# Kernel optimization log

Hardware: AMD Instinct MI355X
Metric: run time of the kernel (lower is better)

The kernel has to match this reference:

```python
import jax, jax.numpy as jnp
import numpy as np

NQ = 16  # nqubits
BATCH = 256

def _ry(t):
    # t: (...,) real angles -> (..., 2, 2) complex64 Ry(t)
    c = jnp.cos(t / 2).astype(jnp.complex64)
    s = jnp.sin(t / 2).astype(jnp.complex64)
    return jnp.stack([jnp.stack([c, -s], -1), jnp.stack([s, c], -1)], -2)

def _rz(t):
    # diag(e^{-i t/2}, e^{i t/2})
    e0 = jnp.exp(-0.5j * t.astype(jnp.complex64))
    e1 = jnp.exp(0.5j * t.astype(jnp.complex64))
    z = jnp.zeros_like(e0)
    return jnp.stack([jnp.stack([e0, z], -1), jnp.stack([z, e1], -1)], -2)

def _apply_1q(st, g, w):
    # st: (B, 2^n) complex, g: (2,2) or (B,2,2); wire w (0 = most significant, matching kron order)
    B = st.shape[0]
    x = st.reshape(B, 2 ** w, 2, -1)
    if g.ndim == 3:
        x = jnp.einsum('iab,ilbr->ilar', g, x)
    else:
        x = jnp.einsum('ab,ilbr->ilar', g, x)
    return x.reshape(B, -1)

def _apply_cnot(st, c, t, n):
    # CNOT(control=c, target=t): flip target bit where control bit == 1
    B = st.shape[0]
    x = st.reshape((B,) + (2,) * n)
    c_ax = c + 1
    ctrl0 = jnp.take(x, 0, axis=c_ax)
    ctrl1 = jnp.take(x, 1, axis=c_ax)
    t_ax = t + 1 if t < c else t  # target axis index after removing control axis
    ctrl1 = jnp.flip(ctrl1, axis=t_ax)  # flip along size-2 axis == Pauli-X
    x = jnp.stack([ctrl0, ctrl1], axis=c_ax)
    return x.reshape(B, -1)

def _yzy(st, w3, n):
    # per-qubit Ry(a) Rz(b) Ry(c); params laid out (n, 3) applied in order a, b, c
    p = w3.reshape(n, 3)
    g = jnp.einsum('nab,nbc,ncd->nad', _ry(p[:, 2]), _rz(p[:, 1]), _ry(p[:, 0]))
    for i in range(n):
        st = _apply_1q(st, g[i], i)
    return st

def _ring(st, step, n):
    # ring_of_cnot (step=1) / ring_of_cnot2 (step=2)
    for i in range(n):
        st = _apply_cnot(st, i, (i + step) % n, n)
    return st

def _forward(inputs, weight):
    B, n = inputs.shape
    # |0...0> initial state, batched
    st = jnp.zeros((B, 2 ** n), jnp.complex64).at[:, 0].set(1.0)
    # PauliEncoding with pauli='Y': Ry(inputs[:, i]) on wire i (batched gate)
    enc = _ry(inputs)  # (B, n, 2, 2)
    for i in range(n):
        st = _apply_1q(st, enc[:, i], i)
    # BasicEntangleLayer x2 = YZY + ring_of_cnot
    st = _yzy(st, weight[0 * n:3 * n], n); st = _ring(st, 1, n)
    st = _yzy(st, weight[3 * n:6 * n], n); st = _ring(st, 1, n)
    # YZY, ring_of_cnot2, YZY, ring_of_cnot2, YZY
    st = _yzy(st, weight[6 * n:9 * n], n); st = _ring(st, 2, n)
    st = _yzy(st, weight[9 * n:12 * n], n); st = _ring(st, 2, n)
    st = _yzy(st, weight[12 * n:15 * n], n)
    # <Z_i> = sum_probs(bit_i=0) - sum_probs(bit_i=1); output scaled by 4 as in original
    probs = st.real ** 2 + st.imag ** 2  # (B, 2^n) real
    z = []
    for i in range(n):
        p = probs.reshape(B, 2 ** i, 2, -1)
        z.append((p[:, :, 0, :] - p[:, :, 1, :]).sum(axis=(1, 2)))
    return jnp.stack(z, axis=1) * 4.0  # (B, n)

def setup_inputs() -> dict:
    key = jax.random.key(0)
    k1, k2 = jax.random.split(key)
    inputs = jax.random.uniform(k1, (BATCH, NQ), jnp.float32, 0.0, 2.0 * np.pi)
    weight = jax.random.uniform(k2, (15 * NQ,), jnp.float32, 0.0, 2.0 * np.pi)
    return {"inputs": inputs, "weight": weight}

def reference(inputs, weight):
    return _forward(inputs, weight)
```

## Files before the change

### kernel.cpp

```cpp
#include <hip/hip_runtime.h>
#include <hip/hip_fp16.h>
#include <utility>
#include <type_traits>


struct M16 { unsigned r[16]; };

constexpr M16 ident() { M16 m{}; for (int i = 0; i < 16; ++i) m.r[i] = 1u << i; return m; }

constexpr M16 ringm(int s) {
  M16 m = ident();
  for (int i = 15; i >= 0; --i) {
    int pc = 15 - i;
    int pt = 15 - ((i + s) & 15);
    m.r[pt] ^= m.r[pc];
  }
  return m;
}

constexpr M16 mmul(M16 A, M16 B) {
  M16 C{};
  for (int p = 0; p < 16; ++p) {
    unsigned v = 0;
    for (int q = 0; q < 16; ++q) if ((A.r[p] >> q) & 1u) v ^= B.r[q];
    C.r[p] = v;
  }
  return C;
}

constexpr M16 minv(M16 A) {
  M16 I = ident();
  for (int col = 0; col < 16; ++col) {
    int piv = -1;
    for (int row = col; row < 16; ++row) if ((A.r[row] >> col) & 1u) { piv = row; break; }
    unsigned t = A.r[piv]; A.r[piv] = A.r[col]; A.r[col] = t;
    t = I.r[piv]; I.r[piv] = I.r[col]; I.r[col] = t;
    for (int row = 0; row < 16; ++row)
      if (row != col && ((A.r[row] >> col) & 1u)) { A.r[row] ^= A.r[col]; I.r[row] ^= I.r[col]; }
  }
  return I;
}

constexpr bool meq(M16 a, M16 b) { for (int i = 0; i < 16; ++i) if (a.r[i] != b.r[i]) return false; return true; }
constexpr unsigned colmask(M16 P, int b) { unsigned m = 0; for (int p = 0; p < 16; ++p) m |= ((P.r[p] >> b) & 1u) << p; return m; }
constexpr int popc16(unsigned x) { int c = 0; for (int i = 0; i < 16; ++i) c += (x >> i) & 1; return c; }
constexpr int topbit_pow(unsigned x) { int b = 0; for (int i = 0; i < 16; ++i) if ((x >> i) & 1) b = i; return 1 << b; }

struct Tables { unsigned gm[64]; unsigned gc[64]; unsigned meas[16]; };

constexpr Tables make_tables() {
  Tables T{};
  M16 R1 = ringm(1), R2 = ringm(2);
  M16 P0 = R1;
  M16 P1 = mmul(R1, R1);
  M16 P2 = mmul(P1, R2);
  M16 P3 = mmul(P2, R2);
  M16 P[4] = { P0, P1, P2, P3 };
  for (int k = 0; k < 4; ++k) {
    M16 A = minv(P[k]);
    for (int b = 0; b < 16; ++b) {
      T.gm[k * 16 + b] = colmask(P[k], b);
      T.gc[k * 16 + b] = A.r[b];
    }
  }
  M16 A5 = minv(P[3]);
  for (int w = 0; w < 16; ++w) T.meas[w] = A5.r[15 - w];
  return T;
}

constexpr Tables TB = make_tables();

constexpr bool check_tables() {
  for (int g = 0; g < 64; ++g) if ((popc16(TB.gm[g] & TB.gc[g]) & 1) != 1) return false;
  if (!meq(mmul(ringm(1), minv(ringm(1))), ident())) return false;
  if (!meq(mmul(ringm(2), minv(ringm(2))), ident())) return false;
  return true;
}
static_assert(check_tables(), "GF(2) table inconsistency");
static_assert(sizeof(__half2) == 4, "half2 size");

template<int N, int I = 0, typename F>
__device__ __forceinline__ void sfor(F&& f) {
  if constexpr (I < N) {
    f(std::integral_constant<int, I>{});
    sfor<N, I + 1>(static_cast<F&&>(f));
  }
}

__device__ __forceinline__ int h2i(__half2 v) { return __builtin_bit_cast(int, v); }
__device__ __forceinline__ __half2 i2h(int v) { return __builtin_bit_cast(__half2, v); }
__device__ __forceinline__ unsigned h2u(__half2 v) { return __builtin_bit_cast(unsigned, v); }
__device__ __forceinline__ __half2 u2h(unsigned v) { return __builtin_bit_cast(__half2, v); }

__device__ __forceinline__ __half2 hswap(__half2 v) { __half2 r; r.x = v.y; r.y = v.x; return r; }

__device__ __forceinline__ __half2 updc(__half2 xs, __half2 xp, const __half2 (&s)[4]) {
  __half2 y = __hmul2(s[0], xs);
  y = __hfma2(s[1], hswap(xs), y);
  y = __hfma2(s[2], xp, y);
  y = __hfma2(s[3], hswap(xp), y);
  return y;
}
template<int T>
__device__ __forceinline__ __half2 upd(__half2 xs, __half2 xp,
                                       const __half2 (&s0)[4], const __half2 (&s1)[4]) {
  if constexpr (T) return updc(xs, xp, s1); else return updc(xs, xp, s0);
}

__device__ __forceinline__ void su2_coeffs(float a, float b, float c,
                                           float& are, float& aim, float& bre, float& bim) {
  float sapc, capc, samc, camc, sb, cb;
  __sincosf((a + c) * 0.5f, &sapc, &capc);
  __sincosf((a - c) * 0.5f, &samc, &camc);
  __sincosf(b * 0.5f, &sb, &cb);
  are = cb * capc;
  aim = -sb * camc;
  bre = cb * sapc;
  bim = sb * samc;
}

__device__ __forceinline__ unsigned pkh2(float lo, float hi) {
  return h2u(__floats2half2_rn(lo, hi));
}

__device__ __forceinline__ float2 cmulf(float2 a, float vr, float vi) {
  return make_float2(a.x * vr - a.y * vi, a.x * vi + a.y * vr);
}

template<int G>
__device__ __forceinline__ void apply_gate(__half2 (&S)[64], unsigned tid,
                                           const unsigned* ctab, unsigned* xbuf) {
  constexpr unsigned m  = TB.gm[G];
  constexpr unsigned c  = TB.gc[G];
  constexpr unsigned mL = m & 63u;
  constexpr unsigned mT = m >> 6;
  constexpr unsigned mW = m >> 12;
  constexpr int      dt = popc16(c & mL) & 1;

  __half2 s0[4], s1[4];
  {
    const unsigned f = __popc((c >> 6) & tid) & 1u;
#pragma unroll
    for (int q = 0; q < 4; ++q) {
      const unsigned lo = ctab[G * 8 + q];
      const unsigned hi = ctab[G * 8 + 4 + q];
      s0[q] = u2h(f ? hi : lo);
      s1[q] = u2h(f ? lo : hi);
    }
  }

  if constexpr (mT == 0u) {
    static_assert(mT != 0u || dt == 1, "register-pair gate must flip role locally");
    constexpr int hb = topbit_pow(mL);
    sfor<32>([&](auto ii) {
      constexpr int i  = decltype(ii)::value;
      constexpr int L0 = ((i & ~(hb - 1)) << 1) | (i & (hb - 1));
      constexpr int L1 = L0 ^ (int)mL;
      constexpr int t  = popc16(c & (unsigned)L0) & 1;
      const __half2 x0 = S[L0], x1 = S[L1];
      S[L0] = upd<t>(x0, x1, s0, s1);
      S[L1] = upd<t ^ dt>(x1, x0, s0, s1);
    });
  } else if constexpr (mW == 0u) {
    if constexpr (mL == 0u) {
      sfor<64>([&](auto ll) {
        constexpr int L = decltype(ll)::value;
        constexpr int t = popc16(c & (unsigned)L) & 1;
        const __half2 xp = i2h(__shfl_xor(h2i(S[L]), (int)mT, 64));
        S[L] = upd<t>(S[L], xp, s0, s1);
      });
    } else {
      constexpr int hb = topbit_pow(mL);
      sfor<32>([&](auto ii) {
        constexpr int i  = decltype(ii)::value;
        constexpr int L0 = ((i & ~(hb - 1)) << 1) | (i & (hb - 1));
        constexpr int L1 = L0 ^ (int)mL;
        constexpr int t  = popc16(c & (unsigned)L0) & 1;
        const __half2 x0 = S[L0], x1 = S[L1];
        const __half2 xp0 = i2h(__shfl_xor(h2i(x1), (int)mT, 64));
        const __half2 xp1 = i2h(__shfl_xor(h2i(x0), (int)mT, 64));
        S[L0] = upd<t>(x0, xp0, s0, s1);
        S[L1] = upd<t ^ dt>(x1, xp1, s0, s1);
      });
    }
  } else {
    constexpr unsigned hc = mL >> 3;
    const unsigned ptid = tid ^ mT;
    if constexpr (hc == 0u) {
      sfor<4>([&](auto gg_) {
        constexpr int g = decltype(gg_)::value;
        sfor<16>([&](auto ss) {
          constexpr int s = decltype(ss)::value;
          xbuf[s * 1024 + tid] = h2u(S[g * 16 + s]);
        });
        __syncthreads();
        sfor<16>([&](auto ss) {
          constexpr int s    = decltype(ss)::value;
          constexpr int L    = g * 16 + s;
          constexpr int slot = (L ^ (int)mL) & 15;
          constexpr int t    = popc16(c & (unsigned)L) & 1;
          const __half2 xp = u2h(xbuf[slot * 1024 + ptid]);
          S[L] = upd<t>(S[L], xp, s0, s1);
        });
        __syncthreads();
      });
    } else {
      constexpr int tb = topbit_pow(hc);
      sfor<8>([&](auto cc) {
        constexpr int cA = decltype(cc)::value;
        if constexpr ((cA & tb) == 0) {
          constexpr int cB = cA ^ (int)hc;
          sfor<8>([&](auto ss) {
            constexpr int s = decltype(ss)::value;
            xbuf[s * 1024 + tid]       = h2u(S[cA * 8 + s]);
            xbuf[(8 + s) * 1024 + tid] = h2u(S[cB * 8 + s]);
          });
          __syncthreads();
          sfor<8>([&](auto ss) {
            constexpr int s = decltype(ss)::value;
            {
              constexpr int L    = cA * 8 + s;
              constexpr int slot = 8 + ((L ^ (int)mL) & 7);
              constexpr int t    = popc16(c & (unsigned)L) & 1;
              const __half2 xp = u2h(xbuf[slot * 1024 + ptid]);
              S[L] = upd<t>(S[L], xp, s0, s1);
            }
            {
              constexpr int L    = cB * 8 + s;
              constexpr int slot = (L ^ (int)mL) & 7;
              constexpr int t    = popc16(c & (unsigned)L) & 1;
              const __half2 xp = u2h(xbuf[slot * 1024 + ptid]);
              S[L] = upd<t>(S[L], xp, s0, s1);
            }
          });
          __syncthreads();
        }
      });
    }
  }
}

__global__ __attribute__((amdgpu_flat_work_group_size(1024, 1024),
                          amdgpu_waves_per_eu(4, 4)))
void qcir_kernel(const float* __restrict__ inputs, const float* __restrict__ weight,
                 float* __restrict__ out) {
  __shared__ unsigned xbuf[24 * 1024];
  __shared__ unsigned ctab[64 * 8];
  __shared__ float4   itab[16];
  __shared__ float    red[16 * 16];

  const unsigned tid = threadIdx.x;
  const unsigned b   = blockIdx.x;

  if (tid < 64) {
    const int g = (int)tid;
    const int k = g >> 4;
    const int bb = g & 15;
    const int w = 15 - bb;
    const int base = 48 * (k + 1) + 3 * w;
    float are, aim, bre, bim;
    su2_coeffs(weight[base], weight[base + 1], weight[base + 2], are, aim, bre, bim);
    ctab[g * 8 + 0] = pkh2(are, are);
    ctab[g * 8 + 1] = pkh2(-aim, aim);
    ctab[g * 8 + 2] = pkh2(-bre, -bre);
    ctab[g * 8 + 3] = pkh2(-bim, bim);
    ctab[g * 8 + 4] = pkh2(are, are);
    ctab[g * 8 + 5] = pkh2(aim, -aim);
    ctab[g * 8 + 6] = pkh2(bre, bre);
    ctab[g * 8 + 7] = pkh2(-bim, bim);
  } else if (tid < 80) {
    const int w = (int)tid - 64;
    const float a = weight[3 * w] + inputs[b * 16 + w];
    float are, aim, bre, bim;
    su2_coeffs(a, weight[3 * w + 1], weight[3 * w + 2], are, aim, bre, bim);
    itab[w] = make_float4(are, aim, bre, bim);
  }
  __syncthreads();

  __half2 S[64];
  float2 P = make_float2(1.f, 0.f);
#pragma unroll
  for (int p = 6; p <= 15; ++p) {
    const int bit = (int)(tid >> (p - 6)) & 1;
    const float4 t = itab[15 - p];
    P = cmulf(P, bit ? t.z : t.x, bit ? t.w : t.y);
  }
  sfor<8>([&](auto hh) {
    constexpr int h = decltype(hh)::value;
    float2 ph = P;
    sfor<3>([&](auto qq) {
      constexpr int q   = decltype(qq)::value;
      constexpr int bit = (h >> q) & 1;
      const float4 t = itab[15 - (3 + q)];
      if constexpr (bit) ph = cmulf(ph, t.z, t.w); else ph = cmulf(ph, t.x, t.y);
    });
    sfor<8>([&](auto ll) {
      constexpr int l = decltype(ll)::value;
      float2 pl = ph;
      sfor<3>([&](auto qq) {
        constexpr int q   = decltype(qq)::value;
        constexpr int bit = (l >> q) & 1;
        const float4 t = itab[15 - q];
        if constexpr (bit) pl = cmulf(pl, t.z, t.w); else pl = cmulf(pl, t.x, t.y);
      });
      S[h * 8 + l] = __floats2half2_rn(pl.x, pl.y);
    });
  });

  sfor<64>([&](auto gg) { apply_gate<decltype(gg)::value>(S, tid, ctab, xbuf); });

  float acc[16];
  sfor<16>([&](auto ww) { acc[decltype(ww)::value] = 0.f; });
  sfor<64>([&](auto ll) {
    constexpr int L = decltype(ll)::value;
    const float re = __low2float(S[L]);
    const float im = __high2float(S[L]);
    const float p = re * re + im * im;
    sfor<16>([&](auto ww) {
      constexpr int w = decltype(ww)::value;
      constexpr int t = popc16(TB.meas[w] & 63u & (unsigned)L) & 1;
      if constexpr (t) acc[w] -= p; else acc[w] += p;
    });
  });
  sfor<16>([&](auto ww) {
    constexpr int w = decltype(ww)::value;
    const unsigned fw = __popc((TB.meas[w] >> 6) & tid) & 1u;
    float z = fw ? -acc[w] : acc[w];
#pragma unroll
    for (int d = 1; d < 64; d <<= 1) z += __shfl_xor(z, d, 64);
    if ((tid & 63u) == 0u) red[(tid >> 6) * 16 + w] = z;
  });
  __syncthreads();
  if (tid < 16) {
    float s = 0.f;
#pragma unroll
    for (int v = 0; v < 16; ++v) s += red[v * 16 + tid];
    out[b * 16 + tid] = 4.f * s;
  }
}

extern "C" void kernel_launch(void* const* d_in, const int* in_sizes, int n_in,
                              void* d_out, int out_size, void* d_ws, size_t ws_size,
                              hipStream_t stream) {
  const float* inputs = (const float*)d_in[0];
  const float* weight = (const float*)d_in[1];
  float* out = (float*)d_out;
  const int B = in_sizes[0] / 16;
  qcir_kernel<<<B, 1024, 0, stream>>>(inputs, weight, out);
}
```

Baseline: 338.8 us.

## Keep 48 amplitudes in registers and spill the last 16 to LDS

The per-thread state drops from 64 register half2 amplitudes to 48. The remaining 16 live in a per-thread LDS region accessed with 128-bit vector loads and stores, and every gate path is extended to handle the LDS-resident part. The gate coefficients shrink to one uint4 per gate, with a sign-flip mask applied by XOR instead of selecting between two coefficient sets. The aim is to cut register pressure and spilling at 1024 threads per block, paid for with extra LDS traffic on every gate.

New measurement: 356.0 us. 5.1% more time.

```diff
diff --git a/kernel.cpp b/kernel.cpp
--- a/kernel.cpp
+++ b/kernel.cpp
@@ -3,6 +3,8 @@
 #include <utility>
 #include <type_traits>
 
+
+constexpr int NREG = 48;
 
 struct M16 { unsigned r[16]; };
 
@@ -94,17 +96,16 @@
 
 __device__ __forceinline__ __half2 hswap(__half2 v) { __half2 r; r.x = v.y; r.y = v.x; return r; }
 
-__device__ __forceinline__ __half2 updc(__half2 xs, __half2 xp, const __half2 (&s)[4]) {
-  __half2 y = __hmul2(s[0], xs);
-  y = __hfma2(s[1], hswap(xs), y);
-  y = __hfma2(s[2], xp, y);
-  y = __hfma2(s[3], hswap(xp), y);
-  return y;
-}
 template<int T>
 __device__ __forceinline__ __half2 upd(__half2 xs, __half2 xp,
-                                       const __half2 (&s0)[4], const __half2 (&s1)[4]) {
-  if constexpr (T) return updc(xs, xp, s1); else return updc(xs, xp, s0);
+                                       __half2 c0, __half2 c1, __half2 c2, __half2 c3) {
+  __half2 c1t = c1, c2t = c2;
+  if constexpr (T) { c1t = __hneg2(c1); c2t = __hneg2(c2); }
+  __half2 y = __hmul2(c0, xs);
+  y = __hfma2(c1t, hswap(xs), y);
+  y = __hfma2(c2t, xp, y);
+  y = __hfma2(c3, hswap(xp), y);
+  return y;
 }
 
 __device__ __forceinline__ void su2_coeffs(float a, float b, float c,
@@ -127,9 +128,72 @@
   return make_float2(a.x * vr - a.y * vi, a.x * vi + a.y * vr);
 }
 
+template<int g4>
+__device__ __forceinline__ void ldg(const uint4* slds4, unsigned tid, __half2 (&a)[4]) {
+  const uint4 v = slds4[g4 * 1024 + tid];
+  a[0] = u2h(v.x); a[1] = u2h(v.y); a[2] = u2h(v.z); a[3] = u2h(v.w);
+}
+template<int g4>
+__device__ __forceinline__ void stg(uint4* slds4, unsigned tid, const __half2 (&a)[4]) {
+  slds4[g4 * 1024 + tid] = make_uint4(h2u(a[0]), h2u(a[1]), h2u(a[2]), h2u(a[3]));
+}
+
+template<int ch, int sb, int NR>
+__device__ __forceinline__ void stage_chunk(const __half2 (&S)[NR], unsigned tid,
+                                            const uint4* slds4, unsigned* xbuf) {
+  if constexpr (ch < 6) {
+    sfor<8>([&](auto kk) {
+      constexpr int k = decltype(kk)::value;
+      xbuf[(sb + k) * 1024 + tid] = h2u(S[ch * 8 + k]);
+    });
+  } else {
+    sfor<2>([&](auto uu) {
+      constexpr int u = decltype(uu)::value;
+      __half2 a[4];
+      ldg<(ch - 6) * 2 + u>(slds4, tid, a);
+      sfor<4>([&](auto ee) {
+        constexpr int e = decltype(ee)::value;
+        xbuf[(sb + u * 4 + e) * 1024 + tid] = h2u(a[e]);
+      });
+    });
+  }
+}
+
+template<int ch, int pb, unsigned mLt, unsigned ct, int NR>
+__device__ __forceinline__ void compute_chunk(__half2 (&S)[NR], unsigned tid, unsigned ptid,
+                                              uint4* slds4, const unsigned* xbuf,
+                                              __half2 c0, __half2 c1, __half2 c2, __half2 c3) {
+  if constexpr (ch < 6) {
+    sfor<8>([&](auto kk) {
+      constexpr int k = decltype(kk)::value;
+      constexpr int L = ch * 8 + k;
+      constexpr int slot = pb + ((L ^ (int)mLt) & 7);
+      constexpr int t = popc16(ct & (unsigned)L) & 1;
+      const __half2 xp = u2h(xbuf[slot * 1024 + ptid]);
+      S[L] = upd<t>(S[L], xp, c0, c1, c2, c3);
+    });
+  } else {
+    sfor<2>([&](auto uu) {
+      constexpr int u = decltype(uu)::value;
+      constexpr int g = (ch - 6) * 2 + u;
+      __half2 a[4];
+      ldg<g>(slds4, tid, a);
+      sfor<4>([&](auto ee) {
+        constexpr int e = decltype(ee)::value;
+        constexpr int L = ch * 8 + u * 4 + e;
+        constexpr int slot = pb + ((L ^ (int)mLt) & 7);
+        constexpr int t = popc16(ct & (unsigned)L) & 1;
+        const __half2 xp = u2h(xbuf[slot * 1024 + ptid]);
+        a[e] = upd<t>(a[e], xp, c0, c1, c2, c3);
+      });
+      stg<g>(slds4, tid, a);
+    });
+  }
+}
+
 template<int G>
-__device__ __forceinline__ void apply_gate(__half2 (&S)[64], unsigned tid,
-                                           const unsigned* ctab, unsigned* xbuf) {
+__device__ __forceinline__ void apply_gate(__half2 (&S)[NREG], unsigned tid,
+                                           const uint4* ctab4, uint4* slds4, unsigned* xbuf) {
   constexpr unsigned m  = TB.gm[G];
   constexpr unsigned c  = TB.gc[G];
   constexpr unsigned mL = m & 63u;
@@ -137,37 +201,106 @@
   constexpr unsigned mW = m >> 12;
   constexpr int      dt = popc16(c & mL) & 1;
 
-  __half2 s0[4], s1[4];
+  __half2 c0, c1, c2, c3;
   {
-    const unsigned f = __popc((c >> 6) & tid) & 1u;
-#pragma unroll
-    for (int q = 0; q < 4; ++q) {
-      const unsigned lo = ctab[G * 8 + q];
-      const unsigned hi = ctab[G * 8 + 4 + q];
-      s0[q] = u2h(f ? hi : lo);
-      s1[q] = u2h(f ? lo : hi);
-    }
-  }
+    const uint4 cc = ctab4[G];
+    const unsigned fm = (__popc((c >> 6) & tid) & 1u) ? 0x80008000u : 0u;
+    c0 = u2h(cc.x); c1 = u2h(cc.y ^ fm); c2 = u2h(cc.z ^ fm); c3 = u2h(cc.w);
+  }
+
+  constexpr unsigned dq = (mL >> 4) & 3u;
+  constexpr unsigned mn = mL & 15u;
 
   if constexpr (mT == 0u) {
-    static_assert(mT != 0u || dt == 1, "register-pair gate must flip role locally");
+    static_assert(dt == 1, "local pair gate must flip role");
     constexpr int hb = topbit_pow(mL);
     sfor<32>([&](auto ii) {
       constexpr int i  = decltype(ii)::value;
       constexpr int L0 = ((i & ~(hb - 1)) << 1) | (i & (hb - 1));
       constexpr int L1 = L0 ^ (int)mL;
-      constexpr int t  = popc16(c & (unsigned)L0) & 1;
-      const __half2 x0 = S[L0], x1 = S[L1];
-      S[L0] = upd<t>(x0, x1, s0, s1);
-      S[L1] = upd<t ^ dt>(x1, x0, s0, s1);
-    });
+      if constexpr (L0 < NREG && L1 < NREG) {
+        constexpr int t = popc16(c & (unsigned)L0) & 1;
+        const __half2 x0 = S[L0], x1 = S[L1];
+        S[L0] = upd<t>(x0, x1, c0, c1, c2, c3);
+        S[L1] = upd<t ^ dt>(x1, x0, c0, c1, c2, c3);
+      }
+    });
+    if constexpr (dq == 0u) {
+      constexpr unsigned hg = mn >> 2;
+      if constexpr (hg == 0u) {
+        constexpr int eb = topbit_pow(mn);
+        sfor<4>([&](auto gg4) {
+          constexpr int g = decltype(gg4)::value;
+          __half2 a[4]; ldg<g>(slds4, tid, a);
+          sfor<2>([&](auto jj) {
+            constexpr int j  = decltype(jj)::value;
+            constexpr int e0 = ((j & ~(eb - 1)) << 1) | (j & (eb - 1));
+            constexpr int e1 = e0 ^ (int)mn;
+            constexpr int L0 = 48 + g * 4 + e0;
+            constexpr int t  = popc16(c & (unsigned)L0) & 1;
+            const __half2 x0 = a[e0], x1 = a[e1];
+            a[e0] = upd<t>(x0, x1, c0, c1, c2, c3);
+            a[e1] = upd<t ^ dt>(x1, x0, c0, c1, c2, c3);
+          });
+          stg<g>(slds4, tid, a);
+        });
+      } else {
+        constexpr int gb = topbit_pow(hg);
+        sfor<2>([&](auto jj) {
+          constexpr int j  = decltype(jj)::value;
+          constexpr int gA = ((j & ~(gb - 1)) << 1) | (j & (gb - 1));
+          constexpr int gB = gA ^ (int)hg;
+          __half2 a[4], bb[4];
+          ldg<gA>(slds4, tid, a); ldg<gB>(slds4, tid, bb);
+          sfor<4>([&](auto ee) {
+            constexpr int e  = decltype(ee)::value;
+            constexpr int e2 = e ^ (int)(mn & 3u);
+            constexpr int L0 = 48 + gA * 4 + e;
+            constexpr int t  = popc16(c & (unsigned)L0) & 1;
+            const __half2 x0 = a[e], x1 = bb[e2];
+            a[e]   = upd<t>(x0, x1, c0, c1, c2, c3);
+            bb[e2] = upd<t ^ dt>(x1, x0, c0, c1, c2, c3);
+          });
+          stg<gA>(slds4, tid, a); stg<gB>(slds4, tid, bb);
+        });
+      }
+    } else {
+      constexpr int qr = 3 ^ (int)dq;
+      sfor<4>([&](auto gg4) {
+        constexpr int g = decltype(gg4)::value;
+        __half2 a[4]; ldg<g>(slds4, tid, a);
+        sfor<4>([&](auto ee) {
+          constexpr int e  = decltype(ee)::value;
+          constexpr int s  = g * 4 + e;
+          constexpr int Lr = (qr << 4) | (s ^ (int)mn);
+          static_assert(Lr < NREG, "reg partner must be register-resident");
+          constexpr int tr = popc16(c & (unsigned)Lr) & 1;
+          const __half2 xr = S[Lr], xl = a[e];
+          S[Lr] = upd<tr>(xr, xl, c0, c1, c2, c3);
+          a[e]  = upd<tr ^ dt>(xl, xr, c0, c1, c2, c3);
+        });
+        stg<g>(slds4, tid, a);
+      });
+    }
   } else if constexpr (mW == 0u) {
     if constexpr (mL == 0u) {
-      sfor<64>([&](auto ll) {
+      sfor<NREG>([&](auto ll) {
         constexpr int L = decltype(ll)::value;
         constexpr int t = popc16(c & (unsigned)L) & 1;
         const __half2 xp = i2h(__shfl_xor(h2i(S[L]), (int)mT, 64));
-        S[L] = upd<t>(S[L], xp, s0, s1);
+        S[L] = upd<t>(S[L], xp, c0, c1, c2, c3);
+      });
+      sfor<4>([&](auto gg4) {
+        constexpr int g = decltype(gg4)::value;
+        __half2 a[4]; ldg<g>(slds4, tid, a);
+        sfor<4>([&](auto ee) {
+          constexpr int e = decltype(ee)::value;
+          constexpr int L = 48 + g * 4 + e;
+          constexpr int t = popc16(c & (unsigned)L) & 1;
+          const __half2 xp = i2h(__shfl_xor(h2i(a[e]), (int)mT, 64));
+          a[e] = upd<t>(a[e], xp, c0, c1, c2, c3);
+        });
+        stg<g>(slds4, tid, a);
       });
     } else {
       constexpr int hb = topbit_pow(mL);
@@ -175,64 +308,138 @@
         constexpr int i  = decltype(ii)::value;
         constexpr int L0 = ((i & ~(hb - 1)) << 1) | (i & (hb - 1));
         constexpr int L1 = L0 ^ (int)mL;
-        constexpr int t  = popc16(c & (unsigned)L0) & 1;
-        const __half2 x0 = S[L0], x1 = S[L1];
-        const __half2 xp0 = i2h(__shfl_xor(h2i(x1), (int)mT, 64));
-        const __half2 xp1 = i2h(__shfl_xor(h2i(x0), (int)mT, 64));
-        S[L0] = upd<t>(x0, xp0, s0, s1);
-        S[L1] = upd<t ^ dt>(x1, xp1, s0, s1);
-      });
+        if constexpr (L0 < NREG && L1 < NREG) {
+          constexpr int t = popc16(c & (unsigned)L0) & 1;
+          const __half2 x0 = S[L0], x1 = S[L1];
+          const __half2 xp0 = i2h(__shfl_xor(h2i(x1), (int)mT, 64));
+          const __half2 xp1 = i2h(__shfl_xor(h2i(x0), (int)mT, 64));
+          S[L0] = upd<t>(x0, xp0, c0, c1, c2, c3);
+          S[L1] = upd<t ^ dt>(x1, xp1, c0, c1, c2, c3);
+        }
+      });
+      if constexpr (dq == 0u) {
+        constexpr unsigned hg = mn >> 2;
+        if constexpr (hg == 0u) {
+          constexpr int eb = topbit_pow(mn);
+          sfor<4>([&](auto gg4) {
+            constexpr int g = decltype(gg4)::value;
+            __half2 a[4]; ldg<g>(slds4, tid, a);
+            sfor<2>([&](auto jj) {
+              constexpr int j  = decltype(jj)::value;
+              constexpr int e0 = ((j & ~(eb - 1)) << 1) | (j & (eb - 1));
+              constexpr int e1 = e0 ^ (int)mn;
+              constexpr int L0 = 48 + g * 4 + e0;
+              constexpr int t  = popc16(c & (unsigned)L0) & 1;
+              const __half2 x0 = a[e0], x1 = a[e1];
+              const __half2 xp0 = i2h(__shfl_xor(h2i(x1), (int)mT, 64));
+              const __half2 xp1 = i2h(__shfl_xor(h2i(x0), (int)mT, 64));
+              a[e0] = upd<t>(x0, xp0, c0, c1, c2, c3);
+              a[e1] = upd<t ^ dt>(x1, xp1, c0, c1, c2, c3);
+            });
+            stg<g>(slds4, tid, a);
+          });
+        } else {
+          constexpr int gb = topbit_pow(hg);
+          sfor<2>([&](auto jj) {
+            constexpr int j  = decltype(jj)::value;
+            constexpr int gA = ((j & ~(gb - 1)) << 1) | (j & (gb - 1));
+            constexpr int gB = gA ^ (int)hg;
+            __half2 a[4], bb[4];
+            ldg<gA>(slds4, tid, a); ldg<gB>(slds4, tid, bb);
+            sfor<4>([&](auto ee) {
+              constexpr int e  = decltype(ee)::value;
+              constexpr int e2 = e ^ (int)(mn & 3u);
+              constexpr int L0 = 48 + gA * 4 + e;
+              constexpr int t  = popc16(c & (unsigned)L0) & 1;
+              const __half2 x0 = a[e], x1 = bb[e2];
+              const __half2 xp0 = i2h(__shfl_xor(h2i(x1), (int)mT, 64));
+              const __half2 xp1 = i2h(__shfl_xor(h2i(x0), (int)mT, 64));
+              a[e]   = upd<t>(x0, xp0, c0, c1, c2, c3);
+              bb[e2] = upd<t ^ dt>(x1, xp1, c0, c1, c2, c3);
+            });
+            stg<gA>(slds4, tid, a); stg<gB>(slds4, tid, bb);
+          });
+        }
+      } else {
+        constexpr int qr = 3 ^ (int)dq;
+        sfor<4>([&](auto gg4) {
+          constexpr int g = decltype(gg4)::value;
+          __half2 a[4]; ldg<g>(slds4, tid, a);
+          sfor<4>([&](auto ee) {
+            constexpr int e  = decltype(ee)::value;
+            constexpr int s  = g * 4 + e;
+            constexpr int Lr = (qr << 4) | (s ^ (int)mn);
+            static_assert(Lr < NREG, "reg partner must be register-resident");
+            constexpr int tr = popc16(c & (unsigned)Lr) & 1;
+            const __half2 xr = S[Lr], xl = a[e];
+            const __half2 xpr = i2h(__shfl_xor(h2i(xl), (int)mT, 64));
+            const __half2 xpl = i2h(__shfl_xor(h2i(xr), (int)mT, 64));
+            S[Lr] = upd<tr>(xr, xpr, c0, c1, c2, c3);
+            a[e]  = upd<tr ^ dt>(xl, xpl, c0, c1, c2, c3);
+          });
+          stg<g>(slds4, tid, a);
+        });
+      }
     }
   } else {
+    const unsigned ptid = tid ^ mT;
     constexpr unsigned hc = mL >> 3;
-    const unsigned ptid = tid ^ mT;
     if constexpr (hc == 0u) {
       sfor<4>([&](auto gg_) {
         constexpr int g = decltype(gg_)::value;
-        sfor<16>([&](auto ss) {
-          constexpr int s = decltype(ss)::value;
-          xbuf[s * 1024 + tid] = h2u(S[g * 16 + s]);
-        });
+        if constexpr (g < 3) {
+          sfor<16>([&](auto ss) {
+            constexpr int s = decltype(ss)::value;
+            xbuf[s * 1024 + tid] = h2u(S[g * 16 + s]);
+          });
+        } else {
+          sfor<4>([&](auto grr) {
+            constexpr int gr = decltype(grr)::value;
+            __half2 a[4]; ldg<gr>(slds4, tid, a);
+            sfor<4>([&](auto ee) {
+              constexpr int e = decltype(ee)::value;
+              xbuf[(gr * 4 + e) * 1024 + tid] = h2u(a[e]);
+            });
+          });
+        }
         __syncthreads();
-        sfor<16>([&](auto ss) {
-          constexpr int s    = decltype(ss)::value;
-          constexpr int L    = g * 16 + s;
-          constexpr int slot = (L ^ (int)mL) & 15;
-          constexpr int t    = popc16(c & (unsigned)L) & 1;
-          const __half2 xp = u2h(xbuf[slot * 1024 + ptid]);
-          S[L] = upd<t>(S[L], xp, s0, s1);
-        });
+        if constexpr (g < 3) {
+          sfor<16>([&](auto ss) {
+            constexpr int s    = decltype(ss)::value;
+            constexpr int L    = g * 16 + s;
+            constexpr int slot = (L ^ (int)mL) & 15;
+            constexpr int t    = popc16(c & (unsigned)L) & 1;
+            const __half2 xp = u2h(xbuf[slot * 1024 + ptid]);
+            S[L] = upd<t>(S[L], xp, c0, c1, c2, c3);
+          });
+        } else {
+          sfor<4>([&](auto grr) {
+            constexpr int gr = decltype(grr)::value;
+            __half2 a[4]; ldg<gr>(slds4, tid, a);
+            sfor<4>([&](auto ee) {
+              constexpr int e    = decltype(ee)::value;
+              constexpr int L    = 48 + gr * 4 + e;
+              constexpr int slot = (L ^ (int)mL) & 15;
+              constexpr int t    = popc16(c & (unsigned)L) & 1;
+              const __half2 xp = u2h(xbuf[slot * 1024 + ptid]);
+              a[e] = upd<t>(a[e], xp, c0, c1, c2, c3);
+            });
+            stg<gr>(slds4, tid, a);
+          });
+        }
         __syncthreads();
       });
     } else {
       constexpr int tb = topbit_pow(hc);
-      sfor<8>([&](auto cc) {
-        constexpr int cA = decltype(cc)::value;
+      sfor<8>([&](auto cc_) {
+        constexpr int cA = decltype(cc_)::value;
         if constexpr ((cA & tb) == 0) {
           constexpr int cB = cA ^ (int)hc;
-          sfor<8>([&](auto ss) {
-            constexpr int s = decltype(ss)::value;
-            xbuf[s * 1024 + tid]       = h2u(S[cA * 8 + s]);
-            xbuf[(8 + s) * 1024 + tid] = h2u(S[cB * 8 + s]);
-          });
+          stage_chunk<cA, 0>(S, tid, slds4, xbuf);
+          stage_chunk<cB, 8>(S, tid, slds4, xbuf);
           __syncthreads();
-          sfor<8>([&](auto ss) {
-            constexpr int s = decltype(ss)::value;
-            {
-              constexpr int L    = cA * 8 + s;
-              constexpr int slot = 8 + ((L ^ (int)mL) & 7);
-              constexpr int t    = popc16(c & (unsigned)L) & 1;
-              const __half2 xp = u2h(xbuf[slot * 1024 + ptid]);
-              S[L] = upd<t>(S[L], xp, s0, s1);
-            }
-            {
-              constexpr int L    = cB * 8 + s;
-              constexpr int slot = (L ^ (int)mL) & 7;
-              constexpr int t    = popc16(c & (unsigned)L) & 1;
-              const __half2 xp = u2h(xbuf[slot * 1024 + ptid]);
-              S[L] = upd<t>(S[L], xp, s0, s1);
-            }
-          });
+          compute_chunk<cA, 8, mL, c>(S, tid, ptid, slds4, xbuf, c0, c1, c2, c3);
+          compute_chunk<cB, 0, mL, c>(S, tid, ptid, slds4, xbuf, c0, c1, c2, c3);
           __syncthreads();
         }
       });
@@ -244,8 +451,9 @@
                           amdgpu_waves_per_eu(4, 4)))
 void qcir_kernel(const float* __restrict__ inputs, const float* __restrict__ weight,
                  float* __restrict__ out) {
-  __shared__ unsigned xbuf[24 * 1024];
-  __shared__ unsigned ctab[64 * 8];
+  __shared__ uint4    slds4[4 * 1024];
+  __shared__ unsigned xbuf[16 * 1024];
+  __shared__ uint4    ctab4[64];
   __shared__ float4   itab[16];
   __shared__ float    red[16 * 16];
 
@@ -260,14 +468,8 @@
     const int base = 48 * (k + 1) + 3 * w;
     float are, aim, bre, bim;
     su2_coeffs(weight[base], weight[base + 1], weight[base + 2], are, aim, bre, bim);
-    ctab[g * 8 + 0] = pkh2(are, are);
-    ctab[g * 8 + 1] = pkh2(-aim, aim);
-    ctab[g * 8 + 2] = pkh2(-bre, -bre);
-    ctab[g * 8 + 3] = pkh2(-bim, bim);
-    ctab[g * 8 + 4] = pkh2(are, are);
-    ctab[g * 8 + 5] = pkh2(aim, -aim);
-    ctab[g * 8 + 6] = pkh2(bre, bre);
-    ctab[g * 8 + 7] = pkh2(-bim, bim);
+    ctab4[g] = make_uint4(pkh2(are, are), pkh2(-aim, aim),
+                          pkh2(-bre, -bre), pkh2(-bim, bim));
   } else if (tid < 80) {
     const int w = (int)tid - 64;
     const float a = weight[3 * w] + inputs[b * 16 + w];
@@ -277,7 +479,7 @@
   }
   __syncthreads();
 
-  __half2 S[64];
+  __half2 S[NREG];
   float2 P = make_float2(1.f, 0.f);
 #pragma unroll
   for (int p = 6; p <= 15; ++p) {
@@ -294,24 +496,42 @@
       const float4 t = itab[15 - (3 + q)];
       if constexpr (bit) ph = cmulf(ph, t.z, t.w); else ph = cmulf(ph, t.x, t.y);
     });
-    sfor<8>([&](auto ll) {
-      constexpr int l = decltype(ll)::value;
-      float2 pl = ph;
-      sfor<3>([&](auto qq) {
-        constexpr int q   = decltype(qq)::value;
-        constexpr int bit = (l >> q) & 1;
-        const float4 t = itab[15 - q];
-        if constexpr (bit) pl = cmulf(pl, t.z, t.w); else pl = cmulf(pl, t.x, t.y);
-      });
-      S[h * 8 + l] = __floats2half2_rn(pl.x, pl.y);
-    });
+    if constexpr (h < 6) {
+      sfor<8>([&](auto ll) {
+        constexpr int l = decltype(ll)::value;
+        float2 pl = ph;
+        sfor<3>([&](auto qq) {
+          constexpr int q   = decltype(qq)::value;
+          constexpr int bit = (l >> q) & 1;
+          const float4 t = itab[15 - q];
+          if constexpr (bit) pl = cmulf(pl, t.z, t.w); else pl = cmulf(pl, t.x, t.y);
+        });
+        S[h * 8 + l] = __floats2half2_rn(pl.x, pl.y);
+      });
+    } else {
+      __half2 a0[4], a1[4];
+      sfor<8>([&](auto ll) {
+        constexpr int l = decltype(ll)::value;
+        float2 pl = ph;
+        sfor<3>([&](auto qq) {
+          constexpr int q   = decltype(qq)::value;
+          constexpr int bit = (l >> q) & 1;
+          const float4 t = itab[15 - q];
+          if constexpr (bit) pl = cmulf(pl, t.z, t.w); else pl = cmulf(pl, t.x, t.y);
+        });
+        const __half2 v = __floats2half2_rn(pl.x, pl.y);
+        if constexpr (l < 4) a0[l] = v; else a1[l - 4] = v;
+      });
+      stg<(h - 6) * 2>(slds4, tid, a0);
+      stg<(h - 6) * 2 + 1>(slds4, tid, a1);
+    }
   });
 
-  sfor<64>([&](auto gg) { apply_gate<decltype(gg)::value>(S, tid, ctab, xbuf); });
+  sfor<64>([&](auto gg) { apply_gate<decltype(gg)::value>(S, tid, ctab4, slds4, xbuf); });
 
   float acc[16];
   sfor<16>([&](auto ww) { acc[decltype(ww)::value] = 0.f; });
-  sfor<64>([&](auto ll) {
+  sfor<NREG>([&](auto ll) {
     constexpr int L = decltype(ll)::value;
     const float re = __low2float(S[L]);
     const float im = __high2float(S[L]);
@@ -320,6 +540,22 @@
       constexpr int w = decltype(ww)::value;
       constexpr int t = popc16(TB.meas[w] & 63u & (unsigned)L) & 1;
       if constexpr (t) acc[w] -= p; else acc[w] += p;
+    });
+  });
+  sfor<4>([&](auto gg4) {
+    constexpr int g = decltype(gg4)::value;
+    __half2 a[4]; ldg<g>(slds4, tid, a);
+    sfor<4>([&](auto ee) {
+      constexpr int e = decltype(ee)::value;
+      constexpr int L = 48 + g * 4 + e;
+      const float re = __low2float(a[e]);
+      const float im = __high2float(a[e]);
+      const float p = re * re + im * im;
+      sfor<16>([&](auto ww) {
+        constexpr int w = decltype(ww)::value;
+        constexpr int t = popc16(TB.meas[w] & 63u & (unsigned)L) & 1;
+        if constexpr (t) acc[w] -= p; else acc[w] += p;
+      });
     });
   });
   sfor<16>([&](auto ww) {
```

## Double per-thread amplitudes, vectorize swizzled LDS exchange, precompute gate coefficients

Applied to the files above, without the earlier changes.

Each block now runs 512 threads, with each thread holding 128 half2 amplitudes instead of 64. More qubits become register-local, and gates that span the whole block need fewer exchange rounds and barriers. Cross-thread exchanges now move uint4 vectors through a swizzled shared buffer, and the per-gate coefficients are built once by a small preceding kernel into global workspace. The sign variants are derived with an XOR mask instead of a second table. The costs are much higher register pressure under launch bounds (512,2), with possible spills, and a 128KB LDS buffer that limits residency to one block per CU.

Result: slower. 367.5 us (+8.5%).

```diff
diff --git a/kernel.cpp b/kernel.cpp
--- a/kernel.cpp
+++ b/kernel.cpp
@@ -94,17 +94,16 @@
 
 __device__ __forceinline__ __half2 hswap(__half2 v) { __half2 r; r.x = v.y; r.y = v.x; return r; }
 
-__device__ __forceinline__ __half2 updc(__half2 xs, __half2 xp, const __half2 (&s)[4]) {
-  __half2 y = __hmul2(s[0], xs);
-  y = __hfma2(s[1], hswap(xs), y);
-  y = __hfma2(s[2], xp, y);
-  y = __hfma2(s[3], hswap(xp), y);
-  return y;
-}
 template<int T>
 __device__ __forceinline__ __half2 upd(__half2 xs, __half2 xp,
-                                       const __half2 (&s0)[4], const __half2 (&s1)[4]) {
-  if constexpr (T) return updc(xs, xp, s1); else return updc(xs, xp, s0);
+                                       __half2 c0, __half2 c1, __half2 c2, __half2 c3) {
+  __half2 c1t = c1, c2t = c2;
+  if constexpr (T) { c1t = __hneg2(c1); c2t = __hneg2(c2); }
+  __half2 y = __hmul2(c0, xs);
+  y = __hfma2(c1t, hswap(xs), y);
+  y = __hfma2(c2t, xp, y);
+  y = __hfma2(c3, hswap(xp), y);
+  return y;
 }
 
 __device__ __forceinline__ void su2_coeffs(float a, float b, float c,
@@ -128,148 +127,153 @@
 }
 
 template<int G>
-__device__ __forceinline__ void apply_gate(__half2 (&S)[64], unsigned tid,
-                                           const unsigned* ctab, unsigned* xbuf) {
+__device__ __forceinline__ void apply_gate(__half2 (&S)[128], unsigned tid,
+                                           const uint4* __restrict__ ctabg,
+                                           uint4* xbuf4) {
   constexpr unsigned m  = TB.gm[G];
   constexpr unsigned c  = TB.gc[G];
-  constexpr unsigned mL = m & 63u;
-  constexpr unsigned mT = m >> 6;
-  constexpr unsigned mW = m >> 12;
+  constexpr unsigned mL = m & 127u;
+  constexpr unsigned mT = m >> 7;
+  constexpr unsigned mW = m >> 13;
   constexpr int      dt = popc16(c & mL) & 1;
 
-  __half2 s0[4], s1[4];
-  {
-    const unsigned f = __popc((c >> 6) & tid) & 1u;
-#pragma unroll
-    for (int q = 0; q < 4; ++q) {
-      const unsigned lo = ctab[G * 8 + q];
-      const unsigned hi = ctab[G * 8 + 4 + q];
-      s0[q] = u2h(f ? hi : lo);
-      s1[q] = u2h(f ? lo : hi);
-    }
-  }
+  const uint4 cc = ctabg[G];
+  const unsigned fm = (__popc((c >> 7) & tid) & 1u) ? 0x80008000u : 0u;
+  const __half2 c0 = u2h(cc.x), c1 = u2h(cc.y ^ fm), c2 = u2h(cc.z ^ fm), c3 = u2h(cc.w);
 
   if constexpr (mT == 0u) {
-    static_assert(mT != 0u || dt == 1, "register-pair gate must flip role locally");
+    static_assert(dt == 1, "local pair gate must flip role");
     constexpr int hb = topbit_pow(mL);
-    sfor<32>([&](auto ii) {
+    sfor<64>([&](auto ii) {
       constexpr int i  = decltype(ii)::value;
       constexpr int L0 = ((i & ~(hb - 1)) << 1) | (i & (hb - 1));
       constexpr int L1 = L0 ^ (int)mL;
       constexpr int t  = popc16(c & (unsigned)L0) & 1;
       const __half2 x0 = S[L0], x1 = S[L1];
-      S[L0] = upd<t>(x0, x1, s0, s1);
-      S[L1] = upd<t ^ dt>(x1, x0, s0, s1);
+      S[L0] = upd<t>(x0, x1, c0, c1, c2, c3);
+      S[L1] = upd<t ^ dt>(x1, x0, c0, c1, c2, c3);
     });
   } else if constexpr (mW == 0u) {
+    constexpr int lx = (int)mT;
     if constexpr (mL == 0u) {
-      sfor<64>([&](auto ll) {
+      sfor<128>([&](auto ll) {
         constexpr int L = decltype(ll)::value;
         constexpr int t = popc16(c & (unsigned)L) & 1;
-        const __half2 xp = i2h(__shfl_xor(h2i(S[L]), (int)mT, 64));
-        S[L] = upd<t>(S[L], xp, s0, s1);
+        const __half2 xp = i2h(__shfl_xor(h2i(S[L]), lx, 64));
+        S[L] = upd<t>(S[L], xp, c0, c1, c2, c3);
       });
     } else {
       constexpr int hb = topbit_pow(mL);
-      sfor<32>([&](auto ii) {
+      sfor<64>([&](auto ii) {
         constexpr int i  = decltype(ii)::value;
         constexpr int L0 = ((i & ~(hb - 1)) << 1) | (i & (hb - 1));
         constexpr int L1 = L0 ^ (int)mL;
         constexpr int t  = popc16(c & (unsigned)L0) & 1;
         const __half2 x0 = S[L0], x1 = S[L1];
-        const __half2 xp0 = i2h(__shfl_xor(h2i(x1), (int)mT, 64));
-        const __half2 xp1 = i2h(__shfl_xor(h2i(x0), (int)mT, 64));
-        S[L0] = upd<t>(x0, xp0, s0, s1);
-        S[L1] = upd<t ^ dt>(x1, xp1, s0, s1);
+        const __half2 xp0 = i2h(__shfl_xor(h2i(x1), lx, 64));
+        const __half2 xp1 = i2h(__shfl_xor(h2i(x0), lx, 64));
+        S[L0] = upd<t>(x0, xp0, c0, c1, c2, c3);
+        S[L1] = upd<t ^ dt>(x1, xp1, c0, c1, c2, c3);
       });
     }
   } else {
-    constexpr unsigned hc = mL >> 3;
-    const unsigned ptid = tid ^ mT;
-    if constexpr (hc == 0u) {
-      sfor<4>([&](auto gg_) {
-        constexpr int g = decltype(gg_)::value;
-        sfor<16>([&](auto ss) {
-          constexpr int s = decltype(ss)::value;
-          xbuf[s * 1024 + tid] = h2u(S[g * 16 + s]);
+    const unsigned ptid = tid ^ (unsigned)mT;
+    const unsigned swz  = tid & 15u;
+    const unsigned pswz = ptid & 15u;
+    constexpr unsigned hc4 = mL >> 2;
+    constexpr int      mn2 = (int)(mL & 3u);
+    if constexpr (hc4 == 0u) {
+      sfor<2>([&](auto it_) {
+        constexpr int it = decltype(it_)::value;
+        sfor<16>([&](auto kk) {
+          constexpr int k = decltype(kk)::value;
+          constexpr int g = it * 16 + k;
+          xbuf4[tid * 16u + ((unsigned)k ^ swz)] =
+            make_uint4(h2u(S[4*g]), h2u(S[4*g+1]), h2u(S[4*g+2]), h2u(S[4*g+3]));
         });
         __syncthreads();
-        sfor<16>([&](auto ss) {
-          constexpr int s    = decltype(ss)::value;
-          constexpr int L    = g * 16 + s;
-          constexpr int slot = (L ^ (int)mL) & 15;
-          constexpr int t    = popc16(c & (unsigned)L) & 1;
-          const __half2 xp = u2h(xbuf[slot * 1024 + ptid]);
-          S[L] = upd<t>(S[L], xp, s0, s1);
+        sfor<16>([&](auto kk) {
+          constexpr int k = decltype(kk)::value;
+          constexpr int g = it * 16 + k;
+          const uint4 pv = xbuf4[ptid * 16u + ((unsigned)k ^ pswz)];
+          const unsigned pa[4] = { pv.x, pv.y, pv.z, pv.w };
+          sfor<4>([&](auto ee) {
+            constexpr int e = decltype(ee)::value;
+            constexpr int L = 4*g + e;
+            constexpr int t = popc16(c & (unsigned)L) & 1;
+            S[L] = upd<t>(S[L], u2h(pa[e ^ mn2]), c0, c1, c2, c3);
+          });
         });
         __syncthreads();
       });
     } else {
-      constexpr int tb = topbit_pow(hc);
-      sfor<8>([&](auto cc) {
-        constexpr int cA = decltype(cc)::value;
-        if constexpr ((cA & tb) == 0) {
-          constexpr int cB = cA ^ (int)hc;
-          sfor<8>([&](auto ss) {
-            constexpr int s = decltype(ss)::value;
-            xbuf[s * 1024 + tid]       = h2u(S[cA * 8 + s]);
-            xbuf[(8 + s) * 1024 + tid] = h2u(S[cB * 8 + s]);
-          });
-          __syncthreads();
-          sfor<8>([&](auto ss) {
-            constexpr int s = decltype(ss)::value;
+      constexpr int tbH = topbit_pow(hc4);
+      sfor<2>([&](auto it_) {
+        constexpr int it = decltype(it_)::value;
+        sfor<8>([&](auto kk) {
+          constexpr int k  = decltype(kk)::value;
+          constexpr int i  = it * 8 + k;
+          constexpr int gA = ((i & ~(tbH - 1)) << 1) | (i & (tbH - 1));
+          constexpr int gB = gA ^ (int)hc4;
+          xbuf4[tid * 16u + ((unsigned)k ^ swz)] =
+            make_uint4(h2u(S[4*gA]), h2u(S[4*gA+1]), h2u(S[4*gA+2]), h2u(S[4*gA+3]));
+          xbuf4[tid * 16u + ((unsigned)(8 + k) ^ swz)] =
+            make_uint4(h2u(S[4*gB]), h2u(S[4*gB+1]), h2u(S[4*gB+2]), h2u(S[4*gB+3]));
+        });
+        __syncthreads();
+        sfor<8>([&](auto kk) {
+          constexpr int k  = decltype(kk)::value;
+          constexpr int i  = it * 8 + k;
+          constexpr int gA = ((i & ~(tbH - 1)) << 1) | (i & (tbH - 1));
+          constexpr int gB = gA ^ (int)hc4;
+          const uint4 pvb = xbuf4[ptid * 16u + ((unsigned)(8 + k) ^ pswz)];
+          const uint4 pva = xbuf4[ptid * 16u + ((unsigned)k ^ pswz)];
+          const unsigned qb[4] = { pvb.x, pvb.y, pvb.z, pvb.w };
+          const unsigned qa[4] = { pva.x, pva.y, pva.z, pva.w };
+          sfor<4>([&](auto ee) {
+            constexpr int e = decltype(ee)::value;
             {
-              constexpr int L    = cA * 8 + s;
-              constexpr int slot = 8 + ((L ^ (int)mL) & 7);
-              constexpr int t    = popc16(c & (unsigned)L) & 1;
-              const __half2 xp = u2h(xbuf[slot * 1024 + ptid]);
-              S[L] = upd<t>(S[L], xp, s0, s1);
+              constexpr int L = 4*gA + e;
+              constexpr int t = popc16(c & (unsigned)L) & 1;
+              S[L] = upd<t>(S[L], u2h(qb[e ^ mn2]), c0, c1, c2, c3);
             }
             {
-              constexpr int L    = cB * 8 + s;
-              constexpr int slot = (L ^ (int)mL) & 7;
-              constexpr int t    = popc16(c & (unsigned)L) & 1;
-              const __half2 xp = u2h(xbuf[slot * 1024 + ptid]);
-              S[L] = upd<t>(S[L], xp, s0, s1);
+              constexpr int L = 4*gB + e;
+              constexpr int t = popc16(c & (unsigned)L) & 1;
+              S[L] = upd<t>(S[L], u2h(qa[e ^ mn2]), c0, c1, c2, c3);
             }
           });
-          __syncthreads();
-        }
+        });
+        __syncthreads();
       });
     }
   }
 }
 
-__global__ __attribute__((amdgpu_flat_work_group_size(1024, 1024),
-                          amdgpu_waves_per_eu(4, 4)))
-void qcir_kernel(const float* __restrict__ inputs, const float* __restrict__ weight,
-                 float* __restrict__ out) {
-  __shared__ unsigned xbuf[24 * 1024];
-  __shared__ unsigned ctab[64 * 8];
-  __shared__ float4   itab[16];
-  __shared__ float    red[16 * 16];
+__global__ void ctab_build(const float* __restrict__ weight, uint4* __restrict__ ctabg) {
+  const int g = (int)threadIdx.x;
+  const int k = g >> 4;
+  const int bb = g & 15;
+  const int w = 15 - bb;
+  const int base = 48 * (k + 1) + 3 * w;
+  float are, aim, bre, bim;
+  su2_coeffs(weight[base], weight[base + 1], weight[base + 2], are, aim, bre, bim);
+  ctabg[g] = make_uint4(pkh2(are, are), pkh2(-aim, aim),
+                        pkh2(-bre, -bre), pkh2(-bim, bim));
+}
+
+__global__ void __launch_bounds__(512, 2)
+qcir_kernel(const float* __restrict__ inputs, const float* __restrict__ weight,
+            float* __restrict__ out, const uint4* __restrict__ ctabg) {
+  __shared__ uint4  xbuf4[512 * 16];
+  __shared__ float4 itab[16];
+  __shared__ float  red[8 * 16];
 
   const unsigned tid = threadIdx.x;
   const unsigned b   = blockIdx.x;
 
-  if (tid < 64) {
-    const int g = (int)tid;
-    const int k = g >> 4;
-    const int bb = g & 15;
-    const int w = 15 - bb;
-    const int base = 48 * (k + 1) + 3 * w;
-    float are, aim, bre, bim;
-    su2_coeffs(weight[base], weight[base + 1], weight[base + 2], are, aim, bre, bim);
-    ctab[g * 8 + 0] = pkh2(are, are);
-    ctab[g * 8 + 1] = pkh2(-aim, aim);
-    ctab[g * 8 + 2] = pkh2(-bre, -bre);
-    ctab[g * 8 + 3] = pkh2(-bim, bim);
-    ctab[g * 8 + 4] = pkh2(are, are);
-    ctab[g * 8 + 5] = pkh2(aim, -aim);
-    ctab[g * 8 + 6] = pkh2(bre, bre);
-    ctab[g * 8 + 7] = pkh2(-bim, bim);
-  } else if (tid < 80) {
-    const int w = (int)tid - 64;
+  if (tid < 16) {
+    const int w = (int)tid;
     const float a = weight[3 * w] + inputs[b * 16 + w];
     float are, aim, bre, bim;
     su2_coeffs(a, weight[3 * w + 1], weight[3 * w + 2], are, aim, bre, bim);
@@ -277,21 +281,21 @@
   }
   __syncthreads();
 
-  __half2 S[64];
+  __half2 S[128];
   float2 P = make_float2(1.f, 0.f);
 #pragma unroll
-  for (int p = 6; p <= 15; ++p) {
-    const int bit = (int)(tid >> (p - 6)) & 1;
+  for (int p = 7; p <= 15; ++p) {
+    const int bit = (int)(tid >> (p - 7)) & 1;
     const float4 t = itab[15 - p];
     P = cmulf(P, bit ? t.z : t.x, bit ? t.w : t.y);
   }
-  sfor<8>([&](auto hh) {
+  sfor<16>([&](auto hh) {
     constexpr int h = decltype(hh)::value;
     float2 ph = P;
-    sfor<3>([&](auto qq) {
+    sfor<4>([&](auto qq) {
       constexpr int q   = decltype(qq)::value;
       constexpr int bit = (h >> q) & 1;
-      const float4 t = itab[15 - (3 + q)];
+      const float4 t = itab[12 - q];
       if constexpr (bit) ph = cmulf(ph, t.z, t.w); else ph = cmulf(ph, t.x, t.y);
     });
     sfor<8>([&](auto ll) {
@@ -307,24 +311,24 @@
     });
   });
 
-  sfor<64>([&](auto gg) { apply_gate<decltype(gg)::value>(S, tid, ctab, xbuf); });
+  sfor<64>([&](auto gg) { apply_gate<decltype(gg)::value>(S, tid, ctabg, xbuf4); });
 
   float acc[16];
   sfor<16>([&](auto ww) { acc[decltype(ww)::value] = 0.f; });
-  sfor<64>([&](auto ll) {
+  sfor<128>([&](auto ll) {
     constexpr int L = decltype(ll)::value;
     const float re = __low2float(S[L]);
     const float im = __high2float(S[L]);
     const float p = re * re + im * im;
     sfor<16>([&](auto ww) {
       constexpr int w = decltype(ww)::value;
-      constexpr int t = popc16(TB.meas[w] & 63u & (unsigned)L) & 1;
+      constexpr int t = popc16(TB.meas[w] & 127u & (unsigned)L) & 1;
       if constexpr (t) acc[w] -= p; else acc[w] += p;
     });
   });
   sfor<16>([&](auto ww) {
     constexpr int w = decltype(ww)::value;
-    const unsigned fw = __popc((TB.meas[w] >> 6) & tid) & 1u;
+    const unsigned fw = __popc((TB.meas[w] >> 7) & tid) & 1u;
     float z = fw ? -acc[w] : acc[w];
 #pragma unroll
     for (int d = 1; d < 64; d <<= 1) z += __shfl_xor(z, d, 64);
@@ -334,7 +338,7 @@
   if (tid < 16) {
     float s = 0.f;
 #pragma unroll
-    for (int v = 0; v < 16; ++v) s += red[v * 16 + tid];
+    for (int v = 0; v < 8; ++v) s += red[v * 16 + tid];
     out[b * 16 + tid] = 4.f * s;
   }
 }
@@ -346,5 +350,7 @@
   const float* weight = (const float*)d_in[1];
   float* out = (float*)d_out;
   const int B = in_sizes[0] / 16;
-  qcir_kernel<<<B, 1024, 0, stream>>>(inputs, weight, out);
-}
+  uint4* ctabg = reinterpret_cast<uint4*>(d_ws);
+  ctab_build<<<1, 64, 0, stream>>>(weight, ctabg);
+  qcir_kernel<<<B, 512, 0, stream>>>(inputs, weight, out, ctabg);
+}
```
